# Kernel optimization log

Measured on AMD Instinct MI355X. Metric: run time of the kernel, lower is better.

The kernel has to match this reference:

```python
import jax, jax.numpy as jnp
import numpy as np

N = 50000      # num_nodes
E = 800000     # num_edges (before self-loops)
IN_C = 128
HID = 64       # per-head channels (concat=False -> heads averaged)
HEADS = 4
OUT_C = 128
NEG_SLOPE = 0.2
EPS = 1e-5


def setup_inputs() -> dict:
    key = jax.random.key(0)
    ks = jax.random.split(key, 12)
    p = lambda k, shape: jax.random.normal(k, shape, dtype=jnp.float32) * 0.1
    inp = {
        "x": jax.random.normal(ks[0], (N, IN_C), dtype=jnp.float32),
        "edge_index": jax.random.randint(ks[1], (2, E), 0, N, dtype=jnp.int32),
        # layer 1 GATConv params
        "W1": p(ks[2], (IN_C, HEADS * HID)),
        "asrc1": p(ks[3], (HEADS, HID)),
        "adst1": p(ks[4], (HEADS, HID)),
        "b1": jnp.zeros((HID,), jnp.float32),
        "g1": jnp.ones((HID,), jnp.float32),
        "be1": jnp.zeros((HID,), jnp.float32),
        # layer 2 GATConv params
        "W2": p(ks[5], (HID, HEADS * HID)),
        "asrc2": p(ks[6], (HEADS, HID)),
        "adst2": p(ks[7], (HEADS, HID)),
        "b2": jnp.zeros((HID,), jnp.float32),
        "g2": jnp.ones((HID,), jnp.float32),
        "be2": jnp.zeros((HID,), jnp.float32),
        # output projection
        "Wo": p(ks[8], (HID, OUT_C)),
        "bo": jnp.zeros((OUT_C,), jnp.float32),
    }
    return inp


def _gat(x, W, asrc, adst, b, src, dst):
    """PyG GATConv (shared lin, concat=False -> mean over heads, + bias)."""
    n = x.shape[0]
    h = (x @ W).reshape(n, HEADS, HID)          # [N,H,C]
    es = jnp.sum(h * asrc, axis=-1)             # [N,H] alpha_src
    ed = jnp.sum(h * adst, axis=-1)             # [N,H] alpha_dst
    e = jax.nn.leaky_relu(es[src] + ed[dst], NEG_SLOPE)  # [E,H]
    # segment softmax over edges grouped by destination node
    emax = jax.ops.segment_max(e, dst, num_segments=n)
    ex = jnp.exp(e - emax[dst])
    den = jax.ops.segment_sum(ex, dst, num_segments=n)
    alpha = ex / den[dst]                       # [E,H]
    msg = h[src] * alpha[:, :, None]            # [E,H,C]
    out = jax.ops.segment_sum(msg, dst, num_segments=n)  # [N,H,C]
    return out.mean(axis=1) + b                 # concat=False -> head mean


def _ln(x, g, b):
    m = x.mean(-1, keepdims=True)
    v = x.var(-1, keepdims=True)
    return (x - m) / jnp.sqrt(v + EPS) * g + b


def reference(x, edge_index, W1, asrc1, adst1, b1, g1, be1,
              W2, asrc2, adst2, b2, g2, be2, Wo, bo):
    n = x.shape[0]
    loop = jnp.arange(n, dtype=edge_index.dtype)   # GATConv add_self_loops=True
    src = jnp.concatenate([edge_index[0], loop])
    dst = jnp.concatenate([edge_index[1], loop])
    h = jax.nn.relu(_ln(_gat(x, W1, asrc1, adst1, b1, src, dst), g1, be1))
    h = jax.nn.relu(_ln(_gat(h, W2, asrc2, adst2, b2, src, dst), g2, be2))
    return h @ Wo + bo
```

## Files before the change

### kernel.cpp

```cpp
#include <hip/hip_runtime.h>

#define NHEADS 4
#define NEG_SLOPE 0.2f
#define EPS_LN 1e-5f
#define POOLCAP 1536
#define BIN_EPB 8192
#define MAX_NS 800

typedef __attribute__((ext_vector_type(8))) short bf16x8;
typedef __attribute__((ext_vector_type(4))) float f32x4;

__global__ __launch_bounds__(256) void k_init_deg(int* __restrict__ deg, int n) {
    int i = blockIdx.x * 256 + threadIdx.x;
    if (i < n) deg[i] = 1;
}

__global__ __launch_bounds__(256) void k_count(const int* __restrict__ dst, int* __restrict__ deg, int e) {
    int i = blockIdx.x * 256 + threadIdx.x;
    if (i < e) atomicAdd(&deg[dst[i]], 1);
}

__global__ __launch_bounds__(256) void k_scan1(const int* __restrict__ deg, int* __restrict__ rs,
                                               int* __restrict__ bsum, int n) {
    __shared__ int tmp[256];
    int tx = threadIdx.x;
    int i = blockIdx.x * 256 + tx;
    int v = (i < n) ? deg[i] : 0;
    tmp[tx] = v;
    __syncthreads();
    for (int off = 1; off < 256; off <<= 1) {
        int t = (tx >= off) ? tmp[tx - off] : 0;
        __syncthreads();
        tmp[tx] += t;
        __syncthreads();
    }
    if (i < n) rs[i] = tmp[tx] - v;
    if (tx == 255) bsum[blockIdx.x] = tmp[255];
}

__global__ __launch_bounds__(256) void k_scan2(int* __restrict__ bsum, int nb) {
    __shared__ int tmp[256];
    int tx = threadIdx.x;
    int v = (tx < nb) ? bsum[tx] : 0;
    tmp[tx] = v;
    __syncthreads();
    for (int off = 1; off < 256; off <<= 1) {
        int t = (tx >= off) ? tmp[tx - off] : 0;
        __syncthreads();
        tmp[tx] += t;
        __syncthreads();
    }
    if (tx < nb) bsum[tx] = tmp[tx] - v;
}

__global__ __launch_bounds__(256) void k_scan3(int* __restrict__ rs, int* __restrict__ cur,
                                               const int* __restrict__ bsum, int n, int total) {
    int i = blockIdx.x * 256 + threadIdx.x;
    if (i < n) {
        int r = rs[i] + bsum[blockIdx.x];
        rs[i] = r;
        cur[i] = r;
    }
    if (i == 0) rs[n] = total;
}

__global__ __launch_bounds__(256) void k_scatter(const int* __restrict__ src, const int* __restrict__ dst,
                                                 int* __restrict__ cur, int* __restrict__ col, int e, int n) {
    int i = blockIdx.x * 256 + threadIdx.x;
    if (i < e + n) {
        int s, d;
        if (i < e) { s = src[i]; d = dst[i]; }
        else       { s = i - e;  d = i - e;  }
        int p = atomicAdd(&cur[d], 1);
        col[p] = s;
    }
}

__device__ __forceinline__ unsigned short cvt_bf16(float x) {
    unsigned u = __float_as_uint(x);
    u += 0x7fffu + ((u >> 16) & 1u);
    return (unsigned short)(u >> 16);
}

__device__ __forceinline__ unsigned pack2_bf16(float a, float b) {
    return (unsigned)cvt_bf16(a) | ((unsigned)cvt_bf16(b) << 16);
}

__device__ __forceinline__ float blo(unsigned u) { return __uint_as_float(u << 16); }
__device__ __forceinline__ float bhi(unsigned u) { return __uint_as_float(u & 0xffff0000u); }

__global__ __launch_bounds__(256) void k_bin(const int* __restrict__ e_src, const int* __restrict__ e_dst,
                                             int* __restrict__ cursor, unsigned* __restrict__ pool,
                                             int E, int NS) {
    __shared__ unsigned staged[BIN_EPB];
    __shared__ unsigned short st_sl[BIN_EPB];
    __shared__ int scnt[MAX_NS], sprefix[MAX_NS], scur[MAX_NS], gbase[MAX_NS];
    __shared__ int tsum[256];
    int t = threadIdx.x;
    int b0 = blockIdx.x * BIN_EPB;
    for (int s = t; s < NS; s += 256) { scnt[s] = 0; scur[s] = 0; }
    __syncthreads();
    for (int k = 0; k < BIN_EPB / 256; k++) {
        int i = b0 + k * 256 + t;
        if (i < E) atomicAdd(&scnt[e_dst[i] >> 6], 1);
    }
    __syncthreads();
    int per = (NS + 255) / 256;
    int s0 = t * per;
    int acc = 0;
    for (int k = 0; k < per; k++) { int idx = s0 + k; if (idx < NS) acc += scnt[idx]; }
    tsum[t] = acc;
    __syncthreads();
    for (int off = 1; off < 256; off <<= 1) {
        int v = (t >= off) ? tsum[t - off] : 0;
        __syncthreads();
        tsum[t] += v;
        __syncthreads();
    }
    int run = (t == 0) ? 0 : tsum[t - 1];
    for (int k = 0; k < per; k++) {
        int idx = s0 + k;
        if (idx < NS) { sprefix[idx] = run; run += scnt[idx]; }
    }
    for (int s = t; s < NS; s += 256)
        gbase[s] = atomicAdd(&cursor[s], scnt[s]);
    __syncthreads();
    for (int k = 0; k < BIN_EPB / 256; k++) {
        int i = b0 + k * 256 + t;
        if (i < E) {
            int d = e_dst[i];
            int s = e_src[i];
            int sl = d >> 6;
            int p = atomicAdd(&scur[sl], 1);
            int pos = sprefix[sl] + p;
            staged[pos] = (unsigned)s | ((unsigned)(d & 63) << 20);
            st_sl[pos] = (unsigned short)sl;
        }
    }
    __syncthreads();
    int ec = E - b0; if (ec > BIN_EPB) ec = BIN_EPB; if (ec < 0) ec = 0;
    for (int i = t; i < ec; i += 256) {
        unsigned e = staged[i];
        int sl = st_sl[i];
        int off = i - sprefix[sl];
        int gp = gbase[sl] + off;
        if (gp < POOLCAP) pool[(size_t)sl * POOLCAP + gp] = e;
    }
}

template <int K>
__global__ __launch_bounds__(256) void k_gemm_gat(const float* __restrict__ A, const float* __restrict__ B,
                                                  const float* __restrict__ asrc, const float* __restrict__ adst,
                                                  unsigned short* __restrict__ Hb16, float* __restrict__ es,
                                                  float* __restrict__ ed, int M) {
    __shared__ unsigned short Bt[128][136];
    __shared__ unsigned short Al[128][72];
    int tid = threadIdx.x;
    int m0 = blockIdx.x * 128;
    int n0 = blockIdx.y * 128;
    {
        int n = tid & 127;
        int kh = tid >> 7;
        int kbeg = kh * (K >> 1);
        int kend = kbeg + (K >> 1);
        const float* bp = B + n0 + n;
#pragma unroll 4
        for (int k = kbeg; k < kend; k += 4) {
            float b0 = bp[(size_t)k * 256];
            float b1 = bp[(size_t)(k + 1) * 256];
            float b2 = bp[(size_t)(k + 2) * 256];
            float b3 = bp[(size_t)(k + 3) * 256];
            uint2 p;
            p.x = pack2_bf16(b0, b1);
            p.y = pack2_bf16(b2, b3);
            *(uint2*)&Bt[n][k] = p;
        }
    }
    int w = tid >> 6, lane = tid & 63;
    int quad = lane >> 4, col16 = lane & 15;
    int rw = (w >> 1) * 64;
    int ch = w & 1;
    int head = blockIdx.y * 2 + ch;
    f32x4 acc[4][4] = {};
    constexpr int KH = (K > 64) ? 2 : 1;
    for (int h = 0; h < KH; h++) {
        __syncthreads();
#pragma unroll
        for (int it = 0; it < 8; it++) {
            int idx = it * 256 + tid;
            int row = idx >> 4;
            int kq = (idx & 15) << 2;
            float4 a4 = make_float4(0.f, 0.f, 0.f, 0.f);
            int gr = m0 + row;
            if (gr < M) a4 = *(const float4*)&A[(size_t)gr * K + h * 64 + kq];
            uint2 p;
            p.x = pack2_bf16(a4.x, a4.y);
            p.y = pack2_bf16(a4.z, a4.w);
            *(uint2*)&Al[row][kq] = p;
        }
        __syncthreads();
#pragma unroll
        for (int c = 0; c < 2; c++) {
            int kbl = c * 32 + quad * 8;
            int kb = h * 64 + kbl;
            bf16x8 afr[4], bfr[4];
#pragma unroll
            for (int i = 0; i < 4; i++)
                afr[i] = *(const bf16x8*)&Al[rw + i * 16 + col16][kbl];
#pragma unroll
            for (int j = 0; j < 4; j++)
                bfr[j] = *(const bf16x8*)&Bt[ch * 64 + j * 16 + col16][kb];
#pragma unroll
            for (int i = 0; i < 4; i++)
#pragma unroll
                for (int j = 0; j < 4; j++)
                    acc[i][j] = __builtin_amdgcn_mfma_f32_16x16x32_bf16(afr[i], bfr[j], acc[i][j], 0, 0, 0);
        }
    }
    int mw = m0 + rw;
    float av[4], dv[4];
#pragma unroll
    for (int j = 0; j < 4; j++) {
        av[j] = asrc[head * 64 + j * 16 + col16];
        dv[j] = adst[head * 64 + j * 16 + col16];
    }
#pragma unroll
    for (int i = 0; i < 4; i++) {
#pragma unroll
        for (int r = 0; r < 4; r++) {
            int m = mw + i * 16 + quad * 4 + r;
            float se = acc[i][0][r] * av[0] + acc[i][1][r] * av[1]
                     + acc[i][2][r] * av[2] + acc[i][3][r] * av[3];
            float sd = acc[i][0][r] * dv[0] + acc[i][1][r] * dv[1]
                     + acc[i][2][r] * dv[2] + acc[i][3][r] * dv[3];
            se += __shfl_xor(se, 1, 64); sd += __shfl_xor(sd, 1, 64);
            se += __shfl_xor(se, 2, 64); sd += __shfl_xor(sd, 2, 64);
            se += __shfl_xor(se, 4, 64); sd += __shfl_xor(sd, 4, 64);
            se += __shfl_xor(se, 8, 64); sd += __shfl_xor(sd, 8, 64);
            if (m < M) {
#pragma unroll
                for (int j = 0; j < 4; j++)
                    Hb16[(size_t)m * 256 + head * 64 + j * 16 + col16] = cvt_bf16(acc[i][j][r]);
                if (col16 == 0) { es[m * 4 + head] = se; ed[m * 4 + head] = sd; }
            }
        }
    }
}

__global__ __launch_bounds__(256) void k_gemm(const float* __restrict__ A, const float* __restrict__ B,
                                              const float* __restrict__ bias, float* __restrict__ C,
                                              int M, int Nn, int K) {
    __shared__ unsigned short Al[128][72];
    __shared__ unsigned short Bt[128][72];
    int tid = threadIdx.x;
    int m0 = blockIdx.x * 128;
    {
        int n = tid & 127;
        int kh = tid >> 7;
        int kbeg = kh * (K >> 1);
        int kend = kbeg + (K >> 1);
        const float* bp = B + n;
        for (int k = kbeg; k < kend; k += 4) {
            float b0 = bp[(size_t)k * Nn];
            float b1 = bp[(size_t)(k + 1) * Nn];
            float b2 = bp[(size_t)(k + 2) * Nn];
            float b3 = bp[(size_t)(k + 3) * Nn];
            uint2 p;
            p.x = pack2_bf16(b0, b1);
            p.y = pack2_bf16(b2, b3);
            *(uint2*)&Bt[n][k] = p;
        }
    }
#pragma unroll
    for (int it = 0; it < 8; it++) {
        int idx = it * 256 + tid;
        int row = idx >> 4;
        int kq = (idx & 15) << 2;
        float4 a4 = make_float4(0.f, 0.f, 0.f, 0.f);
        if (m0 + row < M) a4 = *(const float4*)&A[(size_t)(m0 + row) * 64 + kq];
        uint2 p;
        p.x = pack2_bf16(a4.x, a4.y);
        p.y = pack2_bf16(a4.z, a4.w);
        *(uint2*)&Al[row][kq] = p;
    }
    __syncthreads();
    int w = tid >> 6, lane = tid & 63;
    int quad = lane >> 4, col16 = lane & 15;
    int rw = (w >> 1) * 64;
    int ch = w & 1;
    f32x4 acc[4][4] = {};
    int kc = K >> 5;
    for (int c = 0; c < kc; c++) {
        int kb = c * 32 + quad * 8;
        bf16x8 afr[4], bfr[4];
#pragma unroll
        for (int i = 0; i < 4; i++)
            afr[i] = *(const bf16x8*)&Al[rw + i * 16 + col16][kb];
#pragma unroll
        for (int j = 0; j < 4; j++)
            bfr[j] = *(const bf16x8*)&Bt[ch * 64 + j * 16 + col16][kb];
#pragma unroll
        for (int i = 0; i < 4; i++)
#pragma unroll
            for (int j = 0; j < 4; j++)
                acc[i][j] = __builtin_amdgcn_mfma_f32_16x16x32_bf16(afr[i], bfr[j], acc[i][j], 0, 0, 0);
    }
    int mw = m0 + rw;
    float bv[4];
#pragma unroll
    for (int j = 0; j < 4; j++) bv[j] = bias[ch * 64 + j * 16 + col16];
#pragma unroll
    for (int i = 0; i < 4; i++) {
#pragma unroll
        for (int r = 0; r < 4; r++) {
            int m = mw + i * 16 + quad * 4 + r;
            if (m < M) {
#pragma unroll
                for (int j = 0; j < 4; j++)
                    C[(size_t)m * Nn + ch * 64 + j * 16 + col16] = acc[i][j][r] + bv[j];
            }
        }
    }
}

__global__ __launch_bounds__(512) void k_agg_sliced(const unsigned* __restrict__ Hb, const float* __restrict__ es,
                                                    const float* __restrict__ ed, const unsigned* __restrict__ pool,
                                                    const int* __restrict__ cursor, const float* __restrict__ b,
                                                    const float* __restrict__ g, const float* __restrict__ be,
                                                    float* __restrict__ out, int n) {
    __shared__ unsigned ent[POOLCAP];
    __shared__ int lcnt[64], lbase[65], lcur[64];
    int t = threadIdx.x;
    int sl = blockIdx.x;
    if (t < 64) { lcnt[t] = 0; lcur[t] = 0; }
    __syncthreads();
    int ne = cursor[sl]; if (ne > POOLCAP) ne = POOLCAP;
    for (int i = t; i < ne; i += 512)
        atomicAdd(&lcnt[pool[(size_t)sl * POOLCAP + i] >> 20], 1);
    __syncthreads();
    if (t < 64) {
        int v = lcnt[t];
        int x = v;
        for (int off = 1; off < 64; off <<= 1) {
            int y = __shfl_up(x, off, 64);
            if (t >= off) x += y;
        }
        lbase[t] = x - v;
        if (t == 63) lbase[64] = x;
    }
    __syncthreads();
    for (int i = t; i < ne; i += 512) {
        unsigned e = pool[(size_t)sl * POOLCAP + i];
        int ln = e >> 20;
        int p = atomicAdd(&lcur[ln], 1);
        ent[lbase[ln] + p] = e & 0xFFFFFu;
    }
    __syncthreads();
    int wv = t >> 6, lane = t & 63;
    int slot = lane >> 5;
    int sub = lane & 31;
    int headL = sub >> 3;
    int grp = sub & 7;
    for (int j = 0; j < 8; j++) {
        int ln = wv * 8 + j;
        int node = sl * 64 + ln;
        if (node >= n) continue;
        float edv = ed[node * 4 + headL];
        float acc0, acc1, acc2, acc3, acc4, acc5, acc6, acc7, den;
        if (slot == 0) {
            float eS = es[node * 4 + headL] + edv;
            eS = fmaxf(eS, NEG_SLOPE * eS);
            float wS = __expf(eS);
            const uint4 u = *(const uint4*)&Hb[(size_t)node * 128 + (sub << 2)];
            acc0 = wS * blo(u.x); acc1 = wS * bhi(u.x);
            acc2 = wS * blo(u.y); acc3 = wS * bhi(u.y);
            acc4 = wS * blo(u.z); acc5 = wS * bhi(u.z);
            acc6 = wS * blo(u.w); acc7 = wS * bhi(u.w);
            den = wS;
        } else {
            acc0 = acc1 = acc2 = acc3 = acc4 = acc5 = acc6 = acc7 = 0.f;
            den = 0.f;
        }
        int cntn = lcnt[ln];
        int base = lbase[ln];
        int npairs = (cntn + 1) >> 1;
#pragma unroll 2
        for (int p = 0; p < npairs; p++) {
            int eidx = (p << 1) + slot;
            bool valid = eidx < cntn;
            int ridx = base + (valid ? eidx : 0);
            int s = valid ? (int)ent[ridx] : node;
            float e0 = es[s * 4 + headL] + edv;
            e0 = fmaxf(e0, NEG_SLOPE * e0);
            float wgt = valid ? __expf(e0) : 0.f;
            const uint4 u = *(const uint4*)&Hb[(size_t)s * 128 + (sub << 2)];
            acc0 += wgt * blo(u.x); acc1 += wgt * bhi(u.x);
            acc2 += wgt * blo(u.y); acc3 += wgt * bhi(u.y);
            acc4 += wgt * blo(u.z); acc5 += wgt * bhi(u.z);
            acc6 += wgt * blo(u.w); acc7 += wgt * bhi(u.w);
            den += wgt;
        }
        acc0 += __shfl_xor(acc0, 32, 64); acc1 += __shfl_xor(acc1, 32, 64);
        acc2 += __shfl_xor(acc2, 32, 64); acc3 += __shfl_xor(acc3, 32, 64);
        acc4 += __shfl_xor(acc4, 32, 64); acc5 += __shfl_xor(acc5, 32, 64);
        acc6 += __shfl_xor(acc6, 32, 64); acc7 += __shfl_xor(acc7, 32, 64);
        den += __shfl_xor(den, 32, 64);
        float rd = 1.f / den;
        float v0 = acc0 * rd, v1 = acc1 * rd, v2 = acc2 * rd, v3 = acc3 * rd;
        float v4 = acc4 * rd, v5 = acc5 * rd, v6 = acc6 * rd, v7 = acc7 * rd;
        v0 += __shfl_xor(v0, 8, 64);  v1 += __shfl_xor(v1, 8, 64);
        v2 += __shfl_xor(v2, 8, 64);  v3 += __shfl_xor(v3, 8, 64);
        v4 += __shfl_xor(v4, 8, 64);  v5 += __shfl_xor(v5, 8, 64);
        v6 += __shfl_xor(v6, 8, 64);  v7 += __shfl_xor(v7, 8, 64);
        v0 += __shfl_xor(v0, 16, 64); v1 += __shfl_xor(v1, 16, 64);
        v2 += __shfl_xor(v2, 16, 64); v3 += __shfl_xor(v3, 16, 64);
        v4 += __shfl_xor(v4, 16, 64); v5 += __shfl_xor(v5, 16, 64);
        v6 += __shfl_xor(v6, 16, 64); v7 += __shfl_xor(v7, 16, 64);
        float4 bbA = *(const float4*)&b[grp * 8];
        float4 bbB = *(const float4*)&b[grp * 8 + 4];
        v0 = 0.25f * v0 + bbA.x; v1 = 0.25f * v1 + bbA.y;
        v2 = 0.25f * v2 + bbA.z; v3 = 0.25f * v3 + bbA.w;
        v4 = 0.25f * v4 + bbB.x; v5 = 0.25f * v5 + bbB.y;
        v6 = 0.25f * v6 + bbB.z; v7 = 0.25f * v7 + bbB.w;
        float s1 = v0 + v1 + v2 + v3 + v4 + v5 + v6 + v7;
        float s2 = v0 * v0 + v1 * v1 + v2 * v2 + v3 * v3
                 + v4 * v4 + v5 * v5 + v6 * v6 + v7 * v7;
        s1 += __shfl_xor(s1, 1, 64); s2 += __shfl_xor(s2, 1, 64);
        s1 += __shfl_xor(s1, 2, 64); s2 += __shfl_xor(s2, 2, 64);
        s1 += __shfl_xor(s1, 4, 64); s2 += __shfl_xor(s2, 4, 64);
        float mean = s1 * (1.f / 64.f);
        float var = s2 * (1.f / 64.f) - mean * mean;
        float rinv = rsqrtf(var + EPS_LN);
        if (lane < 8) {
            float4 ggA = *(const float4*)&g[grp * 8];
            float4 ggB = *(const float4*)&g[grp * 8 + 4];
            float4 eeA = *(const float4*)&be[grp * 8];
            float4 eeB = *(const float4*)&be[grp * 8 + 4];
            float4 yA, yB;
            yA.x = fmaxf((v0 - mean) * rinv * ggA.x + eeA.x, 0.f);
            yA.y = fmaxf((v1 - mean) * rinv * ggA.y + eeA.y, 0.f);
            yA.z = fmaxf((v2 - mean) * rinv * ggA.z + eeA.z, 0.f);
            yA.w = fmaxf((v3 - mean) * rinv * ggA.w + eeA.w, 0.f);
            yB.x = fmaxf((v4 - mean) * rinv * ggB.x + eeB.x, 0.f);
            yB.y = fmaxf((v5 - mean) * rinv * ggB.y + eeB.y, 0.f);
            yB.z = fmaxf((v6 - mean) * rinv * ggB.z + eeB.z, 0.f);
            yB.w = fmaxf((v7 - mean) * rinv * ggB.w + eeB.w, 0.f);
            *(float4*)&out[(size_t)node * 64 + grp * 8] = yA;
            *(float4*)&out[(size_t)node * 64 + grp * 8 + 4] = yB;
        }
    }
}

__global__ __launch_bounds__(256) void k_gat_aggregate(const unsigned* __restrict__ Hb, const float* __restrict__ es,
                                                       const float* __restrict__ ed, const int* __restrict__ rs,
                                                       const int* __restrict__ col,
                                                       const float* __restrict__ b,
                                                       const float* __restrict__ g, const float* __restrict__ be,
                                                       float* __restrict__ out, int n) {
    int node = blockIdx.x * 4 + (threadIdx.x >> 6);
    int lane = threadIdx.x & 63;
    if (node >= n) return;
    int head = lane >> 4;
    int cp = lane & 15;
    float edv = ed[node * 4 + head];
    float acc0 = 0.f, acc1 = 0.f, acc2 = 0.f, acc3 = 0.f, den = 0.f;
    int i0 = rs[node], i1 = rs[node + 1];
    int i = i0;
    for (; i + 3 < i1; i += 4) {
        int s0 = col[i], s1 = col[i + 1], s2 = col[i + 2], s3 = col[i + 3];
        float e0 = es[s0 * 4 + head];
        float e1 = es[s1 * 4 + head];
        float e2 = es[s2 * 4 + head];
        float e3 = es[s3 * 4 + head];
        uint2 u0 = *(const uint2*)&Hb[(size_t)s0 * 128 + lane * 2];
        uint2 u1 = *(const uint2*)&Hb[(size_t)s1 * 128 + lane * 2];
        uint2 u2 = *(const uint2*)&Hb[(size_t)s2 * 128 + lane * 2];
        uint2 u3 = *(const uint2*)&Hb[(size_t)s3 * 128 + lane * 2];
        e0 += edv; e1 += edv; e2 += edv; e3 += edv;
        e0 = fmaxf(e0, NEG_SLOPE * e0);
        e1 = fmaxf(e1, NEG_SLOPE * e1);
        e2 = fmaxf(e2, NEG_SLOPE * e2);
        e3 = fmaxf(e3, NEG_SLOPE * e3);
        float w0 = __expf(e0), w1 = __expf(e1), w2 = __expf(e2), w3 = __expf(e3);
        acc0 += w0 * blo(u0.x); acc1 += w0 * bhi(u0.x);
        acc2 += w0 * blo(u0.y); acc3 += w0 * bhi(u0.y);
        acc0 += w1 * blo(u1.x); acc1 += w1 * bhi(u1.x);
        acc2 += w1 * blo(u1.y); acc3 += w1 * bhi(u1.y);
        acc0 += w2 * blo(u2.x); acc1 += w2 * bhi(u2.x);
        acc2 += w2 * blo(u2.y); acc3 += w2 * bhi(u2.y);
        acc0 += w3 * blo(u3.x); acc1 += w3 * bhi(u3.x);
        acc2 += w3 * blo(u3.y); acc3 += w3 * bhi(u3.y);
        den += w0 + w1 + w2 + w3;
    }
    for (; i < i1; i++) {
        int s0 = col[i];
        float e0 = es[s0 * 4 + head] + edv;
        uint2 u0 = *(const uint2*)&Hb[(size_t)s0 * 128 + lane * 2];
        e0 = fmaxf(e0, NEG_SLOPE * e0);
        float w0 = __expf(e0);
        acc0 += w0 * blo(u0.x); acc1 += w0 * bhi(u0.x);
        acc2 += w0 * blo(u0.y); acc3 += w0 * bhi(u0.y);
        den += w0;
    }
    float rd = 1.f / den;
    float r0 = acc0 * rd, r1 = acc1 * rd, r2 = acc2 * rd, r3 = acc3 * rd;
    r0 += __shfl_xor(r0, 16, 64); r1 += __shfl_xor(r1, 16, 64);
    r2 += __shfl_xor(r2, 16, 64); r3 += __shfl_xor(r3, 16, 64);
    r0 += __shfl_xor(r0, 32, 64); r1 += __shfl_xor(r1, 32, 64);
    r2 += __shfl_xor(r2, 32, 64); r3 += __shfl_xor(r3, 32, 64);
    float4 bb = *(const float4*)&b[cp * 4];
    float v0 = 0.25f * r0 + bb.x;
    float v1 = 0.25f * r1 + bb.y;
    float v2 = 0.25f * r2 + bb.z;
    float v3 = 0.25f * r3 + bb.w;
    float s = v0 + v1 + v2 + v3;
    float q = v0 * v0 + v1 * v1 + v2 * v2 + v3 * v3;
    for (int off = 1; off < 16; off <<= 1) {
        s += __shfl_xor(s, off, 64);
        q += __shfl_xor(q, off, 64);
    }
    float mean = s * (1.f / 64.f);
    float var = q * (1.f / 64.f) - mean * mean;
    float rinv = rsqrtf(var + EPS_LN);
    float4 gg = *(const float4*)&g[cp * 4];
    float4 ee = *(const float4*)&be[cp * 4];
    if (head == 0) {
        float4 y;
        y.x = fmaxf((v0 - mean) * rinv * gg.x + ee.x, 0.f);
        y.y = fmaxf((v1 - mean) * rinv * gg.y + ee.y, 0.f);
        y.z = fmaxf((v2 - mean) * rinv * gg.z + ee.z, 0.f);
        y.w = fmaxf((v3 - mean) * rinv * gg.w + ee.w, 0.f);
        *(float4*)&out[(size_t)node * 64 + cp * 4] = y;
    }
}

extern "C" void kernel_launch(void* const* d_in, const int* in_sizes, int n_in,
                              void* d_out, int out_size, void* d_ws, size_t ws_size,
                              hipStream_t stream) {
    const float* x     = (const float*)d_in[0];
    const int*   eidx  = (const int*)d_in[1];
    const float* W1    = (const float*)d_in[2];
    const float* asrc1 = (const float*)d_in[3];
    const float* adst1 = (const float*)d_in[4];
    const float* b1    = (const float*)d_in[5];
    const float* g1    = (const float*)d_in[6];
    const float* be1   = (const float*)d_in[7];
    const float* W2    = (const float*)d_in[8];
    const float* asrc2 = (const float*)d_in[9];
    const float* adst2 = (const float*)d_in[10];
    const float* b2    = (const float*)d_in[11];
    const float* g2    = (const float*)d_in[12];
    const float* be2   = (const float*)d_in[13];
    const float* Wo    = (const float*)d_in[14];
    const float* bo    = (const float*)d_in[15];

    const int N = in_sizes[0] / 128;
    const int E = in_sizes[1] / 2;
    const int* srcp = eidx;
    const int* dstp = eidx + E;

    unsigned* hb   = (unsigned*)d_ws;
    float* h_small = (float*)(hb + (size_t)N * 128);
    float* es      = h_small + (size_t)N * 64;
    float* ed      = es + (size_t)N * 4;
    int* tail      = (int*)(ed + (size_t)N * 4);

    const int nb = (N + 255) / 256;
    const int nwb = (N + 3) / 4;
    const int mt128 = (N + 127) / 128;
    const int NS = (N + 63) >> 6;

    size_t prefix_bytes = (size_t)((char*)tail - (char*)d_ws);
    size_t pool_need = prefix_bytes + (size_t)NS * POOLCAP * 4 + (size_t)NS * 4;

    unsigned* pool = (unsigned*)tail;
    int* cursor = (int*)(pool + (size_t)NS * POOLCAP);

    int* rowstart = nullptr; int* colarr = nullptr;
    bool pooled = (ws_size >= pool_need) && (NS <= MAX_NS);

    if (pooled) {
        hipMemsetAsync(cursor, 0, (size_t)NS * 4, stream);
        k_bin<<<(E + BIN_EPB - 1) / BIN_EPB, 256, 0, stream>>>(srcp, dstp, cursor, pool, E, NS);
    } else {
        int* deg  = tail;
        rowstart  = deg + N;
        int* cur  = rowstart + (N + 1);
        colarr    = cur + N;
        int* bsum = colarr + (size_t)(E + N);
        k_init_deg<<<nb, 256, 0, stream>>>(deg, N);
        k_count<<<(E + 255) / 256, 256, 0, stream>>>(dstp, deg, E);
        k_scan1<<<nb, 256, 0, stream>>>(deg, rowstart, bsum, N);
        k_scan2<<<1, 256, 0, stream>>>(bsum, nb);
        k_scan3<<<nb, 256, 0, stream>>>(rowstart, cur, bsum, N, E + N);
        k_scatter<<<(E + N + 255) / 256, 256, 0, stream>>>(srcp, dstp, cur, colarr, E, N);
    }

    k_gemm_gat<128><<<dim3(mt128, 2), 256, 0, stream>>>(x, W1, asrc1, adst1,
                                                        (unsigned short*)hb, es, ed, N);
    if (pooled)
        k_agg_sliced<<<NS, 512, 0, stream>>>(hb, es, ed, pool, cursor, b1, g1, be1, h_small, N);
    else
        k_gat_aggregate<<<nwb, 256, 0, stream>>>(hb, es, ed, rowstart, colarr, b1, g1, be1, h_small, N);

    k_gemm_gat<64><<<dim3(mt128, 2), 256, 0, stream>>>(h_small, W2, asrc2, adst2,
                                                       (unsigned short*)hb, es, ed, N);
    if (pooled)
        k_agg_sliced<<<NS, 512, 0, stream>>>(hb, es, ed, pool, cursor, b2, g2, be2, h_small, N);
    else
        k_gat_aggregate<<<nwb, 256, 0, stream>>>(hb, es, ed, rowstart, colarr, b2, g2, be2, h_small, N);

    k_gemm<<<mt128, 256, 0, stream>>>(h_small, Wo, bo, (float*)d_out, N, 128, 64);
}
```

Before: 340.3 us.

## Fuse aggregation, LayerNorm and next-layer GEMM into one sliced kernel

Adds a templated kernel that aggregates each 64-node slice, applies bias, LayerNorm and ReLU, stages the result as bf16 in shared memory, and runs the next projection (W2 with attention-logit epilogue, or Wo with bias) with MFMA inside the same block. This removes the separate GEMM launches and the global round trip of the intermediate hidden state. The layer-1 projection is written into the output buffer as scratch to save workspace. In exchange, every block reloads and converts the weight matrix into shared memory, and shared memory use grows, which may lower occupancy. The unused CSR fallback path also loses its 4-way unrolled loop.

```diff
diff --git a/kernel.cpp b/kernel.cpp
--- a/kernel.cpp
+++ b/kernel.cpp
@@ -323,6 +323,228 @@
     }
 }
 
+template <int NCOL, bool GAT_EPI>
+__global__ __launch_bounds__(512) void k_agg_fused(const unsigned* __restrict__ Hb_in,
+                                                   const float* __restrict__ es_in,
+                                                   const float* __restrict__ ed_in,
+                                                   const unsigned* __restrict__ pool,
+                                                   const int* __restrict__ cursor,
+                                                   const float* __restrict__ bpre,
+                                                   const float* __restrict__ gln,
+                                                   const float* __restrict__ bln,
+                                                   const float* __restrict__ W,
+                                                   const float* __restrict__ asrc,
+                                                   const float* __restrict__ adst,
+                                                   const float* __restrict__ bout,
+                                                   unsigned short* __restrict__ Hb_out,
+                                                   float* __restrict__ es_out,
+                                                   float* __restrict__ ed_out,
+                                                   float* __restrict__ out_final, int n) {
+    __shared__ unsigned ent[POOLCAP];
+    __shared__ int lcnt[64], lbase[65], lcur[64];
+    __shared__ unsigned short yb[64][72];
+    __shared__ unsigned short Wt[NCOL][72];
+    int t = threadIdx.x;
+    int sl = blockIdx.x;
+    for (int i = t; i < 64 * 36; i += 512) ((unsigned*)yb)[i] = 0u;
+    {
+        constexpr int TPC = 512 / NCOL;
+        constexpr int KPT = 64 / TPC;
+        int nn = t % NCOL;
+        int kh = t / NCOL;
+        const float* wp = W + nn;
+        for (int k = kh * KPT; k < kh * KPT + KPT; k += 4) {
+            float w0 = wp[(size_t)k * NCOL];
+            float w1 = wp[(size_t)(k + 1) * NCOL];
+            float w2 = wp[(size_t)(k + 2) * NCOL];
+            float w3 = wp[(size_t)(k + 3) * NCOL];
+            uint2 p;
+            p.x = pack2_bf16(w0, w1);
+            p.y = pack2_bf16(w2, w3);
+            *(uint2*)&Wt[nn][k] = p;
+        }
+    }
+    if (t < 64) { lcnt[t] = 0; lcur[t] = 0; }
+    __syncthreads();
+    int ne = cursor[sl]; if (ne > POOLCAP) ne = POOLCAP;
+    for (int i = t; i < ne; i += 512)
+        atomicAdd(&lcnt[pool[(size_t)sl * POOLCAP + i] >> 20], 1);
+    __syncthreads();
+    if (t < 64) {
+        int v = lcnt[t], x = v;
+        for (int off = 1; off < 64; off <<= 1) {
+            int y = __shfl_up(x, off, 64);
+            if (t >= off) x += y;
+        }
+        lbase[t] = x - v;
+        if (t == 63) lbase[64] = x;
+    }
+    __syncthreads();
+    for (int i = t; i < ne; i += 512) {
+        unsigned e = pool[(size_t)sl * POOLCAP + i];
+        int ln = e >> 20;
+        int p = atomicAdd(&lcur[ln], 1);
+        ent[lbase[ln] + p] = e & 0xFFFFFu;
+    }
+    __syncthreads();
+    int wv = t >> 6, lane = t & 63;
+    int slot = lane >> 5;
+    int sub = lane & 31;
+    int headL = sub >> 3;
+    int grp = sub & 7;
+    for (int j = 0; j < 8; j++) {
+        int ln = wv * 8 + j;
+        int node = sl * 64 + ln;
+        if (node >= n) continue;
+        float edv = ed_in[node * 4 + headL];
+        float acc0, acc1, acc2, acc3, acc4, acc5, acc6, acc7, den;
+        if (slot == 0) {
+            float eS = es_in[node * 4 + headL] + edv;
+            eS = fmaxf(eS, NEG_SLOPE * eS);
+            float wS = __expf(eS);
+            const uint4 u = *(const uint4*)&Hb_in[(size_t)node * 128 + (sub << 2)];
+            acc0 = wS * blo(u.x); acc1 = wS * bhi(u.x);
+            acc2 = wS * blo(u.y); acc3 = wS * bhi(u.y);
+            acc4 = wS * blo(u.z); acc5 = wS * bhi(u.z);
+            acc6 = wS * blo(u.w); acc7 = wS * bhi(u.w);
+            den = wS;
+        } else {
+            acc0 = acc1 = acc2 = acc3 = acc4 = acc5 = acc6 = acc7 = 0.f;
+            den = 0.f;
+        }
+        int cntn = lcnt[ln];
+        int base = lbase[ln];
+        int npairs = (cntn + 1) >> 1;
+#pragma unroll 2
+        for (int p = 0; p < npairs; p++) {
+            int eidx = (p << 1) + slot;
+            bool valid = eidx < cntn;
+            int s = valid ? (int)ent[base + (valid ? eidx : 0)] : node;
+            float e0 = es_in[s * 4 + headL] + edv;
+            e0 = fmaxf(e0, NEG_SLOPE * e0);
+            float wgt = valid ? __expf(e0) : 0.f;
+            const uint4 u = *(const uint4*)&Hb_in[(size_t)s * 128 + (sub << 2)];
+            acc0 += wgt * blo(u.x); acc1 += wgt * bhi(u.x);
+            acc2 += wgt * blo(u.y); acc3 += wgt * bhi(u.y);
+            acc4 += wgt * blo(u.z); acc5 += wgt * bhi(u.z);
+            acc6 += wgt * blo(u.w); acc7 += wgt * bhi(u.w);
+            den += wgt;
+        }
+        acc0 += __shfl_xor(acc0, 32, 64); acc1 += __shfl_xor(acc1, 32, 64);
+        acc2 += __shfl_xor(acc2, 32, 64); acc3 += __shfl_xor(acc3, 32, 64);
+        acc4 += __shfl_xor(acc4, 32, 64); acc5 += __shfl_xor(acc5, 32, 64);
+        acc6 += __shfl_xor(acc6, 32, 64); acc7 += __shfl_xor(acc7, 32, 64);
+        den += __shfl_xor(den, 32, 64);
+        float rd = 1.f / den;
+        float v0 = acc0 * rd, v1 = acc1 * rd, v2 = acc2 * rd, v3 = acc3 * rd;
+        float v4 = acc4 * rd, v5 = acc5 * rd, v6 = acc6 * rd, v7 = acc7 * rd;
+        v0 += __shfl_xor(v0, 8, 64);  v1 += __shfl_xor(v1, 8, 64);
+        v2 += __shfl_xor(v2, 8, 64);  v3 += __shfl_xor(v3, 8, 64);
+        v4 += __shfl_xor(v4, 8, 64);  v5 += __shfl_xor(v5, 8, 64);
+        v6 += __shfl_xor(v6, 8, 64);  v7 += __shfl_xor(v7, 8, 64);
+        v0 += __shfl_xor(v0, 16, 64); v1 += __shfl_xor(v1, 16, 64);
+        v2 += __shfl_xor(v2, 16, 64); v3 += __shfl_xor(v3, 16, 64);
+        v4 += __shfl_xor(v4, 16, 64); v5 += __shfl_xor(v5, 16, 64);
+        v6 += __shfl_xor(v6, 16, 64); v7 += __shfl_xor(v7, 16, 64);
+        float4 bbA = *(const float4*)&bpre[grp * 8];
+        float4 bbB = *(const float4*)&bpre[grp * 8 + 4];
+        v0 = 0.25f * v0 + bbA.x; v1 = 0.25f * v1 + bbA.y;
+        v2 = 0.25f * v2 + bbA.z; v3 = 0.25f * v3 + bbA.w;
+        v4 = 0.25f * v4 + bbB.x; v5 = 0.25f * v5 + bbB.y;
+        v6 = 0.25f * v6 + bbB.z; v7 = 0.25f * v7 + bbB.w;
+        float s1 = v0 + v1 + v2 + v3 + v4 + v5 + v6 + v7;
+        float s2 = v0 * v0 + v1 * v1 + v2 * v2 + v3 * v3
+                 + v4 * v4 + v5 * v5 + v6 * v6 + v7 * v7;
+        s1 += __shfl_xor(s1, 1, 64); s2 += __shfl_xor(s2, 1, 64);
+        s1 += __shfl_xor(s1, 2, 64); s2 += __shfl_xor(s2, 2, 64);
+        s1 += __shfl_xor(s1, 4, 64); s2 += __shfl_xor(s2, 4, 64);
+        float mean = s1 * (1.f / 64.f);
+        float var = s2 * (1.f / 64.f) - mean * mean;
+        float rinv = rsqrtf(var + EPS_LN);
+        if (lane < 8) {
+            float4 ggA = *(const float4*)&gln[grp * 8];
+            float4 ggB = *(const float4*)&gln[grp * 8 + 4];
+            float4 eeA = *(const float4*)&bln[grp * 8];
+            float4 eeB = *(const float4*)&bln[grp * 8 + 4];
+            float y0 = fmaxf((v0 - mean) * rinv * ggA.x + eeA.x, 0.f);
+            float y1 = fmaxf((v1 - mean) * rinv * ggA.y + eeA.y, 0.f);
+            float y2 = fmaxf((v2 - mean) * rinv * ggA.z + eeA.z, 0.f);
+            float y3 = fmaxf((v3 - mean) * rinv * ggA.w + eeA.w, 0.f);
+            float y4 = fmaxf((v4 - mean) * rinv * ggB.x + eeB.x, 0.f);
+            float y5 = fmaxf((v5 - mean) * rinv * ggB.y + eeB.y, 0.f);
+            float y6 = fmaxf((v6 - mean) * rinv * ggB.z + eeB.z, 0.f);
+            float y7 = fmaxf((v7 - mean) * rinv * ggB.w + eeB.w, 0.f);
+            *(unsigned*)&yb[ln][grp * 8 + 0] = pack2_bf16(y0, y1);
+            *(unsigned*)&yb[ln][grp * 8 + 2] = pack2_bf16(y2, y3);
+            *(unsigned*)&yb[ln][grp * 8 + 4] = pack2_bf16(y4, y5);
+            *(unsigned*)&yb[ln][grp * 8 + 6] = pack2_bf16(y6, y7);
+        }
+    }
+    __syncthreads();
+    constexpr int NT = NCOL / 32;
+    int quad = lane >> 4, col16 = lane & 15;
+    int rw4 = (wv & 3) * 16;
+    int cb = (wv >> 2) * (NCOL / 2);
+    f32x4 acc[NT] = {};
+#pragma unroll
+    for (int c = 0; c < 2; c++) {
+        int kb = c * 32 + quad * 8;
+        bf16x8 afr = *(const bf16x8*)&yb[rw4 + col16][kb];
+#pragma unroll
+        for (int jj = 0; jj < NT; jj++) {
+            bf16x8 bfr = *(const bf16x8*)&Wt[cb + jj * 16 + col16][kb];
+            acc[jj] = __builtin_amdgcn_mfma_f32_16x16x32_bf16(afr, bfr, acc[jj], 0, 0, 0);
+        }
+    }
+    if constexpr (GAT_EPI) {
+        float av[NT], dv[NT];
+#pragma unroll
+        for (int jj = 0; jj < NT; jj++) {
+            av[jj] = asrc[cb + jj * 16 + col16];
+            dv[jj] = adst[cb + jj * 16 + col16];
+        }
+        int headA = cb >> 6;
+#pragma unroll
+        for (int r = 0; r < 4; r++) {
+            int node = sl * 64 + rw4 + quad * 4 + r;
+            float seA = acc[0][r] * av[0] + acc[1][r] * av[1] + acc[2][r] * av[2] + acc[3][r] * av[3];
+            float sdA = acc[0][r] * dv[0] + acc[1][r] * dv[1] + acc[2][r] * dv[2] + acc[3][r] * dv[3];
+            float seB = acc[4][r] * av[4] + acc[5][r] * av[5] + acc[6][r] * av[6] + acc[7][r] * av[7];
+            float sdB = acc[4][r] * dv[4] + acc[5][r] * dv[5] + acc[6][r] * dv[6] + acc[7][r] * dv[7];
+            seA += __shfl_xor(seA, 1, 64); sdA += __shfl_xor(sdA, 1, 64);
+            seB += __shfl_xor(seB, 1, 64); sdB += __shfl_xor(sdB, 1, 64);
+            seA += __shfl_xor(seA, 2, 64); sdA += __shfl_xor(sdA, 2, 64);
+            seB += __shfl_xor(seB, 2, 64); sdB += __shfl_xor(sdB, 2, 64);
+            seA += __shfl_xor(seA, 4, 64); sdA += __shfl_xor(sdA, 4, 64);
+            seB += __shfl_xor(seB, 4, 64); sdB += __shfl_xor(sdB, 4, 64);
+            seA += __shfl_xor(seA, 8, 64); sdA += __shfl_xor(sdA, 8, 64);
+            seB += __shfl_xor(seB, 8, 64); sdB += __shfl_xor(sdB, 8, 64);
+            if (node < n) {
+#pragma unroll
+                for (int jj = 0; jj < NT; jj++)
+                    Hb_out[(size_t)node * 256 + cb + jj * 16 + col16] = cvt_bf16(acc[jj][r]);
+                if (col16 == 0) {
+                    es_out[node * 4 + headA] = seA;     ed_out[node * 4 + headA] = sdA;
+                    es_out[node * 4 + headA + 1] = seB; ed_out[node * 4 + headA + 1] = sdB;
+                }
+            }
+        }
+    } else {
+        float bv[NT];
+#pragma unroll
+        for (int jj = 0; jj < NT; jj++) bv[jj] = bout[cb + jj * 16 + col16];
+#pragma unroll
+        for (int r = 0; r < 4; r++) {
+            int node = sl * 64 + rw4 + quad * 4 + r;
+            if (node < n) {
+#pragma unroll
+                for (int jj = 0; jj < NT; jj++)
+                    out_final[(size_t)node * NCOL + cb + jj * 16 + col16] = acc[jj][r] + bv[jj];
+            }
+        }
+    }
+}
+
 __global__ __launch_bounds__(512) void k_agg_sliced(const unsigned* __restrict__ Hb, const float* __restrict__ es,
                                                     const float* __restrict__ ed, const unsigned* __restrict__ pool,
                                                     const int* __restrict__ cursor, const float* __restrict__ b,
@@ -339,8 +561,7 @@
         atomicAdd(&lcnt[pool[(size_t)sl * POOLCAP + i] >> 20], 1);
     __syncthreads();
     if (t < 64) {
-        int v = lcnt[t];
-        int x = v;
+        int v = lcnt[t], x = v;
         for (int off = 1; off < 64; off <<= 1) {
             int y = __shfl_up(x, off, 64);
             if (t >= off) x += y;
@@ -388,8 +609,7 @@
         for (int p = 0; p < npairs; p++) {
             int eidx = (p << 1) + slot;
             bool valid = eidx < cntn;
-            int ridx = base + (valid ? eidx : 0);
-            int s = valid ? (int)ent[ridx] : node;
+            int s = valid ? (int)ent[base + (valid ? eidx : 0)] : node;
             float e0 = es[s * 4 + headL] + edv;
             e0 = fmaxf(e0, NEG_SLOPE * e0);
             float wgt = valid ? __expf(e0) : 0.f;
@@ -465,34 +685,7 @@
     float edv = ed[node * 4 + head];
     float acc0 = 0.f, acc1 = 0.f, acc2 = 0.f, acc3 = 0.f, den = 0.f;
     int i0 = rs[node], i1 = rs[node + 1];
-    int i = i0;
-    for (; i + 3 < i1; i += 4) {
-        int s0 = col[i], s1 = col[i + 1], s2 = col[i + 2], s3 = col[i + 3];
-        float e0 = es[s0 * 4 + head];
-        float e1 = es[s1 * 4 + head];
-        float e2 = es[s2 * 4 + head];
-        float e3 = es[s3 * 4 + head];
-        uint2 u0 = *(const uint2*)&Hb[(size_t)s0 * 128 + lane * 2];
-        uint2 u1 = *(const uint2*)&Hb[(size_t)s1 * 128 + lane * 2];
-        uint2 u2 = *(const uint2*)&Hb[(size_t)s2 * 128 + lane * 2];
-        uint2 u3 = *(const uint2*)&Hb[(size_t)s3 * 128 + lane * 2];
-        e0 += edv; e1 += edv; e2 += edv; e3 += edv;
-        e0 = fmaxf(e0, NEG_SLOPE * e0);
-        e1 = fmaxf(e1, NEG_SLOPE * e1);
-        e2 = fmaxf(e2, NEG_SLOPE * e2);
-        e3 = fmaxf(e3, NEG_SLOPE * e3);
-        float w0 = __expf(e0), w1 = __expf(e1), w2 = __expf(e2), w3 = __expf(e3);
-        acc0 += w0 * blo(u0.x); acc1 += w0 * bhi(u0.x);
-        acc2 += w0 * blo(u0.y); acc3 += w0 * bhi(u0.y);
-        acc0 += w1 * blo(u1.x); acc1 += w1 * bhi(u1.x);
-        acc2 += w1 * blo(u1.y); acc3 += w1 * bhi(u1.y);
-        acc0 += w2 * blo(u2.x); acc1 += w2 * bhi(u2.x);
-        acc2 += w2 * blo(u2.y); acc3 += w2 * bhi(u2.y);
-        acc0 += w3 * blo(u3.x); acc1 += w3 * bhi(u3.x);
-        acc2 += w3 * blo(u3.y); acc3 += w3 * bhi(u3.y);
-        den += w0 + w1 + w2 + w3;
-    }
-    for (; i < i1; i++) {
+    for (int i = i0; i < i1; i++) {
         int s0 = col[i];
         float e0 = es[s0 * 4 + head] + edv;
         uint2 u0 = *(const uint2*)&Hb[(size_t)s0 * 128 + lane * 2];
@@ -559,16 +752,44 @@
     const int* srcp = eidx;
     const int* dstp = eidx + E;
 
+    const int nb = (N + 255) / 256;
+    const int nwb = (N + 3) / 4;
+    const int mt128 = (N + 127) / 128;
+    const int NS = (N + 63) >> 6;
+
+    unsigned* hb2_f = (unsigned*)d_ws;
+    float* es1_f = (float*)(hb2_f + (size_t)N * 128);
+    float* ed1_f = es1_f + (size_t)N * 4;
+    float* es2_f = ed1_f + (size_t)N * 4;
+    float* ed2_f = es2_f + (size_t)N * 4;
+    unsigned* pool_f = (unsigned*)(ed2_f + (size_t)N * 4);
+    int* cursor_f = (int*)(pool_f + (size_t)NS * POOLCAP);
+    size_t fused_need = (size_t)((char*)(cursor_f + NS) - (char*)d_ws);
+    bool fused = (ws_size >= fused_need) && (NS <= MAX_NS) &&
+                 ((size_t)out_size >= (size_t)N * 512);
+
+    if (fused) {
+        unsigned* hb1 = (unsigned*)d_out;
+        hipMemsetAsync(cursor_f, 0, (size_t)NS * 4, stream);
+        k_bin<<<(E + BIN_EPB - 1) / BIN_EPB, 256, 0, stream>>>(srcp, dstp, cursor_f, pool_f, E, NS);
+        k_gemm_gat<128><<<dim3(mt128, 2), 256, 0, stream>>>(x, W1, asrc1, adst1,
+                                                            (unsigned short*)hb1, es1_f, ed1_f, N);
+        k_agg_fused<256, true><<<NS, 512, 0, stream>>>(hb1, es1_f, ed1_f, pool_f, cursor_f,
+                                                       b1, g1, be1, W2, asrc2, adst2, nullptr,
+                                                       (unsigned short*)hb2_f, es2_f, ed2_f,
+                                                       nullptr, N);
+        k_agg_fused<128, false><<<NS, 512, 0, stream>>>(hb2_f, es2_f, ed2_f, pool_f, cursor_f,
+                                                        b2, g2, be2, Wo, nullptr, nullptr, bo,
+                                                        nullptr, nullptr, nullptr,
+                                                        (float*)d_out, N);
+        return;
+    }
+
     unsigned* hb   = (unsigned*)d_ws;
     float* h_small = (float*)(hb + (size_t)N * 128);
     float* es      = h_small + (size_t)N * 64;
     float* ed      = es + (size_t)N * 4;
     int* tail      = (int*)(ed + (size_t)N * 4);
-
-    const int nb = (N + 255) / 256;
-    const int nwb = (N + 3) / 4;
-    const int mt128 = (N + 127) / 128;
-    const int NS = (N + 63) >> 6;
 
     size_t prefix_bytes = (size_t)((char*)tail - (char*)d_ws);
     size_t pool_need = prefix_bytes + (size_t)NS * POOLCAP * 4 + (size_t)NS * 4;
```

Result: no change. 337.4 us (-0.8%).
